# Performance work log

Hardware: AMD Instinct MI355X
Metric: run time of the kernel (lower is better)

The kernel has to match this reference:

```python
import jax, jax.numpy as jnp
import numpy as np

B, N, F, H, R = 16, 64, 64, 4, 50
C = F * H  # n_coefficients = n_heads * hidden_features
CUTOFF = 5.0  # ExpNormalSmearing cutoff_upper (cutoff_lower = 0)


def _dense(k, fin, fout):
    s = 1.0 / np.sqrt(fin)
    return jax.random.uniform(k, (fin, fout), jnp.float32, -s, s)


def setup_inputs() -> dict:
    key = jax.random.key(0)
    ks = jax.random.split(key, 20)
    start = float(np.exp(-CUTOFF))
    return {
        "h": jax.random.normal(ks[0], (B, N, F), jnp.float32),
        "x": jax.random.normal(ks[1], (B, N, 3), jnp.float32),
        "v": jax.random.normal(ks[2], (B, N, 3), jnp.float32) * 0.1,
        # edge model (ContinuousFilterConvolutionWithConcatenation)
        "W_in": _dense(ks[3], 2 * F, R), "b_in": jnp.zeros((R,), jnp.float32),
        "rbf_means": jnp.linspace(start, 1.0, R).astype(jnp.float32),
        "rbf_betas": jnp.full((R,), (2.0 / R * (1.0 - start)) ** -2, jnp.float32),
        "W_e1": _dense(ks[4], 2 * F + R + 1, F), "b_e1": jnp.zeros((F,), jnp.float32),
        "W_e2": _dense(ks[5], F, F), "b_e2": jnp.zeros((F,), jnp.float32),
        # semantic attention
        "W_sem": _dense(ks[6], F, H), "b_sem": jnp.zeros((H,), jnp.float32),
        "log_gamma": -jnp.log(jnp.linspace(1.0, 5.0, H)).astype(jnp.float32),
        # spatial attention
        "W_xmix": _dense(ks[7], C, C),
        "W_post1": _dense(ks[8], C, F), "b_post1": jnp.zeros((F,), jnp.float32),
        "W_post2": _dense(ks[9], F, F), "b_post2": jnp.zeros((F,), jnp.float32),
        # node update
        "W_node1": _dense(ks[10], F + C + F, F), "b_node1": jnp.zeros((F,), jnp.float32),
        "W_node2": _dense(ks[11], F, F), "b_node2": jnp.zeros((F,), jnp.float32),
        # velocity update
        "W_vel1": _dense(ks[12], F, F), "b_vel1": jnp.zeros((F,), jnp.float32),
        "W_vel2": _dense(ks[13], F, 1),
        "W_vmix": _dense(ks[14], C, 1),
    }


def reference(h, x, v, W_in, b_in, rbf_means, rbf_betas, W_e1, b_e1, W_e2, b_e2,
              W_sem, b_sem, log_gamma, W_xmix, W_post1, b_post1, W_post2, b_post2,
              W_node1, b_node1, W_node2, b_node2, W_vel1, b_vel1, W_vel2, W_vmix):
    silu = jax.nn.silu
    n = h.shape[-2]
    # pairwise displacement x_j - x_i : (B, N, N, 3)
    x_minus_xt = x[..., None, :, :] - x[..., :, None, :]
    d = jnp.sqrt(jax.nn.relu((x_minus_xt ** 2).sum(-1, keepdims=True)) + 1e-5)  # (B,N,N,1)
    # pairwise node features [h_j, h_i] : (B, N, N, 2F)
    hj = jnp.broadcast_to(h[..., None, :, :], h.shape[:-2] + (n, n, h.shape[-1]))
    hi = jnp.broadcast_to(h[..., :, None, :], hj.shape)
    h_cat = jnp.concatenate([hj, hi], -1)
    # edge model: RBF-smeared continuous-filter conv with concatenation
    h_mid = h_cat @ W_in + b_in  # (B,N,N,R)
    cut = 0.5 * (jnp.cos(d * (jnp.pi / CUTOFF)) + 1.0) * (d < CUTOFF)
    rbf = cut * jnp.exp(-rbf_betas * (jnp.exp(-d) - rbf_means) ** 2)  # (B,N,N,R)
    h_e = jnp.concatenate([h_cat, rbf * h_mid, d], -1)
    h_e = silu(h_e @ W_e1 + b_e1) @ W_e2 + b_e2  # (B,N,N,F)
    # attentions, softmax over neighbor axis (-2), diagonal masked out
    eye = jnp.eye(n, dtype=h.dtype)[:, :, None]
    sem = jax.nn.celu(h_e @ W_sem + b_sem, alpha=2.0) - 1e5 * eye
    sem = jax.nn.softmax(sem, axis=-2)  # (B,N,N,H)
    euc = jax.nn.softmax(-(d + 1e5 * eye) * jnp.exp(log_gamma), axis=-2)  # (B,N,N,H)
    att = euc * sem
    att = att / att.sum(-2, keepdims=True)
    # per-head attention-weighted edge features, flattened (F outer, H inner)
    h_e_att = (h_e[..., :, None] * att[..., None, :]).reshape(att.shape[:-1] + (F * H,))
    # spatial attention on unit displacement vectors
    coeff = jnp.tanh(h_e_att @ W_xmix)  # (B,N,N,C)
    x_hat = x_minus_xt / (d + 1e-5)
    comb = x_hat[..., None, :] * coeff[..., None]  # (B,N,N,C,3)
    comb_sum = comb.mean(axis=-3)  # mean over neighbors -> (B,N,C,3)
    h_comb = (comb_sum ** 2).sum(-1)  # invariant squared norms (B,N,C)
    h_comb = silu(silu(h_comb @ W_post1 + b_post1) @ W_post2 + b_post2)
    # node update (residual)
    h_agg = h_e_att.sum(axis=-2)  # (B,N,C)
    h_out = h + silu(silu(jnp.concatenate([h, h_agg, h_comb], -1) @ W_node1 + b_node1) @ W_node2 + b_node2)
    # equivariant velocity / coordinate update
    delta_v = jnp.einsum('...ijcd,c->...id', comb, W_vmix[:, 0]) / n  # v_mixing + mean over j
    gate = 2.0 * jax.nn.sigmoid(silu(h_out @ W_vel1 + b_vel1) @ W_vel2)  # double_sigmoid, (B,N,1)
    v_out = delta_v + gate * v
    x_out = x + v_out
    return h_out, x_out, v_out
```

## Files before the change

kernel.cpp:

```cpp
#include <hip/hip_runtime.h>
#include <math.h>

#define NB 16
#define NN 64
#define NF 64
#define NH 4
#define NR 50
#define NC 256

typedef __attribute__((ext_vector_type(8))) short short8;
typedef __attribute__((ext_vector_type(4))) float f32x4;

#define WS_WE1R 0
#define WS_WE2  4096
#define WS_WX   8192
#define MID_F   36864
#define E1_F    (MID_F + 131072)
#define HAGG_F  (E1_F + 131072)
#define COMB_F  (HAGG_F + 262144)

__device__ __forceinline__ float siluf(float x) { return x / (1.f + __expf(-x)); }
__device__ __forceinline__ float tanhfast(float x) { return 1.f - 2.f / (__expf(2.f * x) + 1.f); }

__device__ __forceinline__ short f2bfs(float f) {
    __bf16 b = (__bf16)f;
    union { __bf16 b; short s; } u; u.b = b; return u.s;
}
__device__ __forceinline__ float bf1(ushort u) {
    union { unsigned u; float f; } c; c.u = ((unsigned)u) << 16; return c.f;
}
__device__ __forceinline__ float bflo(unsigned u) {
    union { unsigned u; float f; } c; c.u = u << 16; return c.f;
}
__device__ __forceinline__ float bfhi(unsigned u) {
    union { unsigned u; float f; } c; c.u = u & 0xFFFF0000u; return c.f;
}

__device__ __forceinline__ float wave_max(float v) {
#pragma unroll
    for (int s = 32; s >= 1; s >>= 1) v = fmaxf(v, __shfl_xor(v, s));
    return v;
}
__device__ __forceinline__ float wave_sum(float v) {
#pragma unroll
    for (int s = 32; s >= 1; s >>= 1) v += __shfl_xor(v, s);
    return v;
}

__global__ __launch_bounds__(256)
void prep_kernel(const float* __restrict__ W_e1, const float* __restrict__ b_e1,
                 const float* __restrict__ W_e2, const float* __restrict__ W_xmix,
                 const float* __restrict__ h, const float* __restrict__ W_in,
                 const float* __restrict__ b_in,
                 short* __restrict__ wpack, float* __restrict__ mid, float* __restrict__ e1)
{
    int blk = blockIdx.x, t = threadIdx.x;
    if (blk < 36) {
        int s = blk * 256 + t;
        short8 val;
        if (s < 512) {
            int cl = s & 15, g = (s >> 4) & 3, q = s >> 6;
            int ks = q & 1, nt = q >> 1;
            int c = nt * 16 + cl, k0 = 32 * ks + 8 * g;
#pragma unroll
            for (int i = 0; i < 8; i++) {
                int kr = k0 + i;
                float f = (kr < 50) ? W_e1[(128 + kr) * NF + c] : (kr == 50 ? W_e1[178 * NF + c] : 0.f);
                val[i] = f2bfs(f);
            }
            *(short8*)(&wpack[WS_WE1R + s * 8]) = val;
        } else if (s < 1024) {
            int u = s - 512;
            int cl = u & 15, g = (u >> 4) & 3, q = u >> 6;
            int ks = q & 1, nt = q >> 1;
            int c = nt * 16 + cl, k0 = 32 * ks + 8 * g;
#pragma unroll
            for (int i = 0; i < 8; i++) val[i] = f2bfs(W_e2[(k0 + i) * NF + c]);
            *(short8*)(&wpack[WS_WE2 + u * 8]) = val;
        } else {
            int u = s - 1024;
            int cl = u & 15, g = (u >> 4) & 3, q = u >> 6;
            int ks = q & 7, wn = q >> 3;
            int c = (wn >> 2) * 64 + (wn & 3) * 16 + cl, k0 = 32 * ks + 8 * g;
#pragma unroll
            for (int i = 0; i < 8; i++) val[i] = f2bfs(W_xmix[(k0 + i) * NC + c]);
            *(short8*)(&wpack[WS_WX + u * 8]) = val;
        }
    } else {
        int node = blk - 36;
        __shared__ float s_hn[64];
        if (t < 64) s_hn[t] = h[node * NF + t];
        __syncthreads();
        if (t < 64) {
            float acc = 0.f;
#pragma unroll 8
            for (int k = 0; k < 64; k++) acc += s_hn[k] * W_e1[k * NF + t];
            e1[node * 128 + t] = acc;
        } else if (t < 128) {
            int f = t - 64;
            float acc = b_e1[f];
#pragma unroll 8
            for (int k = 0; k < 64; k++) acc += s_hn[k] * W_e1[(64 + k) * NF + f];
            e1[node * 128 + 64 + f] = acc;
        } else if (t < 178) {
            int r = t - 128;
            float acc = 0.f;
#pragma unroll 8
            for (int k = 0; k < 64; k++) acc += s_hn[k] * W_in[k * NR + r];
            mid[node * 128 + r] = acc;
        } else if (t >= 192 && t < 242) {
            int r = t - 192;
            float acc = b_in[r];
#pragma unroll 8
            for (int k = 0; k < 64; k++) acc += s_hn[k] * W_in[(64 + k) * NR + r];
            mid[node * 128 + 64 + r] = acc;
        }
    }
}

__global__ __launch_bounds__(256)
void sake_edge_kernel(
    const float* __restrict__ x,
    const float* __restrict__ mid, const float* __restrict__ e1,
    const float* __restrict__ rbf_means, const float* __restrict__ rbf_betas,
    const float* __restrict__ b_e2,
    const float* __restrict__ W_sem, const float* __restrict__ b_sem,
    const float* __restrict__ log_gamma,
    const short* __restrict__ wpack,
    float* __restrict__ hagg_g, float* __restrict__ comb_g)
{
    const int bi = blockIdx.x;
    const int b  = bi >> 6;
    const int i  = bi & 63;
    const int t  = threadIdx.x;
    const int w  = t >> 6, l = t & 63, lr = l & 15, lg = l >> 4;

    __shared__ __align__(16) short s_A[16 * 64 * 8];
    __shared__ short s_he[64 * 66];
    __shared__ float s_xhat[256];
    __shared__ float s_att[256];
    __shared__ float s_wsem[256];
    __shared__ float s_midi[52];

    const short8* A8  = (const short8*)s_A;
    short8*       A8w = (short8*)s_A;
    const short8* We1p = (const short8*)(wpack + WS_WE1R);
    const short8* We2p = (const short8*)(wpack + WS_WE2);
    const short8* Wxp  = (const short8*)(wpack + WS_WX);

    s_wsem[t] = W_sem[t];
    if (t < 50) s_midi[t] = mid[(b * 64 + i) * 128 + 64 + t];
    if (t < 64) {
        int j = t;
        float dx = x[(b * NN + j) * 3 + 0] - x[(b * NN + i) * 3 + 0];
        float dy = x[(b * NN + j) * 3 + 1] - x[(b * NN + i) * 3 + 1];
        float dz = x[(b * NN + j) * 3 + 2] - x[(b * NN + i) * 3 + 2];
        float d2 = dx * dx + dy * dy + dz * dz;
        float d  = sqrtf(fmaxf(d2, 0.f) + 1e-5f);
        float inv = 1.f / (d + 1e-5f);
        s_xhat[j * 4 + 0] = dx * inv;
        s_xhat[j * 4 + 1] = dy * inv;
        s_xhat[j * 4 + 2] = dz * inv;
        s_xhat[j * 4 + 3] = d;
    }
    __syncthreads();

    {
        int j = t & 63, p = t >> 6;
        float d = s_xhat[j * 4 + 3];
        float cut = 0.5f * (__cosf(d * 0.6283185307179586f) + 1.f) * (d < 5.f ? 1.f : 0.f);
        float emd = __expf(-d);
        const float* midj = mid + (b * 64 + j) * 128;
#pragma unroll
        for (int q = 0; q < 2; q++) {
            int sl = 2 * p + q;
            short8 val;
#pragma unroll
            for (int e = 0; e < 8; e++) {
                int r = sl * 8 + e;
                float o;
                if (r < 50) {
                    float m = midj[r] + s_midi[r];
                    float df = emd - rbf_means[r];
                    o = cut * __expf(-rbf_betas[r] * df * df) * m;
                } else if (r == 50) o = d;
                else o = 0.f;
                val[e] = f2bfs(o);
            }
            A8w[sl * 64 + j] = val;
        }
    }
    __syncthreads();

    {
        int f = w * 16 + lr;
        const float* e1b = e1 + (size_t)b * 64 * 128;
        float e1i_v = e1b[i * 128 + 64 + f];
        f32x4 acc[4];
#pragma unroll
        for (int jt = 0; jt < 4; jt++)
#pragma unroll
            for (int r = 0; r < 4; r++) {
                int j = jt * 16 + lg * 4 + r;
                acc[jt][r] = e1b[j * 128 + f] + e1i_v;
            }
#pragma unroll
        for (int ks = 0; ks < 2; ks++) {
            short8 bb = We1p[(w * 2 + ks) * 64 + l];
#pragma unroll
            for (int jt = 0; jt < 4; jt++) {
                short8 aa = A8[(ks * 4 + lg) * 64 + jt * 16 + lr];
                acc[jt] = __builtin_amdgcn_mfma_f32_16x16x32_bf16(aa, bb, acc[jt], 0, 0, 0);
            }
        }
        __syncthreads();
#pragma unroll
        for (int jt = 0; jt < 4; jt++)
#pragma unroll
            for (int r = 0; r < 4; r++) {
                int j = jt * 16 + lg * 4 + r;
                s_A[((f >> 3) * 64 + j) * 8 + (f & 7)] = f2bfs(siluf(acc[jt][r]));
            }
        __syncthreads();
    }

    {
        f32x4 acc[4];
#pragma unroll
        for (int jt = 0; jt < 4; jt++) { acc[jt][0] = 0.f; acc[jt][1] = 0.f; acc[jt][2] = 0.f; acc[jt][3] = 0.f; }
#pragma unroll
        for (int ks = 0; ks < 2; ks++) {
            short8 bb = We2p[(w * 2 + ks) * 64 + l];
#pragma unroll
            for (int jt = 0; jt < 4; jt++) {
                short8 aa = A8[(ks * 4 + lg) * 64 + jt * 16 + lr];
                acc[jt] = __builtin_amdgcn_mfma_f32_16x16x32_bf16(aa, bb, acc[jt], 0, 0, 0);
            }
        }
        float be2 = b_e2[w * 16 + lr];
        int f = w * 16 + lr;
#pragma unroll
        for (int jt = 0; jt < 4; jt++)
#pragma unroll
            for (int r = 0; r < 4; r++) {
                int j = jt * 16 + lg * 4 + r;
                s_he[j * 66 + f] = f2bfs(acc[jt][r] + be2);
            }
        __syncthreads();
    }

    {
        int hh = w, j = l;
        float acc = b_sem[hh];
        const unsigned* hp = (const unsigned*)(s_he + j * 66);
#pragma unroll 8
        for (int q = 0; q < 32; q++) {
            unsigned u = hp[q];
            acc += bflo(u) * s_wsem[(2 * q) * 4 + hh] + bfhi(u) * s_wsem[(2 * q + 1) * 4 + hh];
        }
        float cel = fmaxf(acc, 0.f) + fminf(0.f, 2.f * (__expf(0.5f * acc) - 1.f));
        float diag = (j == i) ? 1e5f : 0.f;
        float slog = cel - diag;
        float m1 = wave_max(slog);
        float e1v = __expf(slog - m1);
        float sem = e1v / wave_sum(e1v);
        float gam = __expf(log_gamma[hh]);
        float elog = -(s_xhat[j * 4 + 3] + diag) * gam;
        float m2 = wave_max(elog);
        float e2 = __expf(elog - m2);
        float euc = e2 / wave_sum(e2);
        float a = sem * euc;
        a = a / wave_sum(a);
        s_att[j * 4 + hh] = a;
    }
    __syncthreads();

    {
        int f = t >> 2, hh = t & 3;
        float acc = 0.f;
#pragma unroll 8
        for (int j = 0; j < 64; j++) acc += bf1((ushort)s_he[j * 66 + f]) * s_att[j * 4 + hh];
        hagg_g[bi * 256 + t] = acc;
    }

    f32x4 acc[4][4];
#pragma unroll
    for (int jt = 0; jt < 4; jt++)
#pragma unroll
        for (int nt = 0; nt < 4; nt++) { acc[jt][nt][0] = 0.f; acc[jt][nt][1] = 0.f; acc[jt][nt][2] = 0.f; acc[jt][nt][3] = 0.f; }

    for (int half = 0; half < 2; half++) {
        {
            int j = t & 63, kc = t >> 6;
            float a0 = s_att[j * 4 + 0], a1 = s_att[j * 4 + 1];
            float a2 = s_att[j * 4 + 2], a3 = s_att[j * 4 + 3];
#pragma unroll
            for (int s = 0; s < 4; s++) {
                int sl = kc * 4 + s;
                int kbase = half * 128 + sl * 8;
                unsigned u = *(const unsigned*)(s_he + j * 66 + (kbase >> 2));
                float h0 = bflo(u), h1 = bfhi(u);
                short8 val;
                val[0] = f2bfs(h0 * a0); val[1] = f2bfs(h0 * a1);
                val[2] = f2bfs(h0 * a2); val[3] = f2bfs(h0 * a3);
                val[4] = f2bfs(h1 * a0); val[5] = f2bfs(h1 * a1);
                val[6] = f2bfs(h1 * a2); val[7] = f2bfs(h1 * a3);
                A8w[sl * 64 + j] = val;
            }
        }
        __syncthreads();
#pragma unroll
        for (int ks = 0; ks < 4; ks++) {
            short8 aa[4], bb[4];
#pragma unroll
            for (int jt = 0; jt < 4; jt++) aa[jt] = A8[(ks * 4 + lg) * 64 + jt * 16 + lr];
#pragma unroll
            for (int nt = 0; nt < 4; nt++) bb[nt] = Wxp[((w * 4 + nt) * 8 + half * 4 + ks) * 64 + l];
#pragma unroll
            for (int jt = 0; jt < 4; jt++)
#pragma unroll
                for (int nt = 0; nt < 4; nt++)
                    acc[jt][nt] = __builtin_amdgcn_mfma_f32_16x16x32_bf16(aa[jt], bb[nt], acc[jt][nt], 0, 0, 0);
        }
        __syncthreads();
    }

    {
#pragma unroll
        for (int nt = 0; nt < 4; nt++) {
            float p0 = 0.f, p1 = 0.f, p2 = 0.f;
#pragma unroll
            for (int jt = 0; jt < 4; jt++)
#pragma unroll
                for (int r = 0; r < 4; r++) {
                    int j = jt * 16 + lg * 4 + r;
                    float th = tanhfast(acc[jt][nt][r]);
                    p0 += s_xhat[j * 4 + 0] * th;
                    p1 += s_xhat[j * 4 + 1] * th;
                    p2 += s_xhat[j * 4 + 2] * th;
                }
            p0 += __shfl_xor(p0, 16); p0 += __shfl_xor(p0, 32);
            p1 += __shfl_xor(p1, 16); p1 += __shfl_xor(p1, 32);
            p2 += __shfl_xor(p2, 16); p2 += __shfl_xor(p2, 32);
            if (lg == 0) {
                int c = w * 64 + nt * 16 + lr;
                float* cg = comb_g + bi * 768 + c * 3;
                cg[0] = p0 * (1.f / 64.f);
                cg[1] = p1 * (1.f / 64.f);
                cg[2] = p2 * (1.f / 64.f);
            }
        }
    }
}

__global__ __launch_bounds__(256)
void sake_tail_kernel(
    const float* __restrict__ h, const float* __restrict__ x, const float* __restrict__ v,
    const float* __restrict__ hagg_g, const float* __restrict__ comb_g,
    const float* __restrict__ W_post1, const float* __restrict__ b_post1,
    const float* __restrict__ W_post2, const float* __restrict__ b_post2,
    const float* __restrict__ W_node1, const float* __restrict__ b_node1,
    const float* __restrict__ W_node2, const float* __restrict__ b_node2,
    const float* __restrict__ W_vel1, const float* __restrict__ b_vel1,
    const float* __restrict__ W_vel2, const float* __restrict__ W_vmix,
    float* __restrict__ out_h, float* __restrict__ out_x, float* __restrict__ out_v)
{
    const int node = blockIdx.x;
    const int t = threadIdx.x, w = t >> 6, l = t & 63;

    __shared__ float s_in[384];
    __shared__ float s_hcp[256];
    __shared__ float s_cmb[3][256];
    __shared__ float s_red[4][64];
    __shared__ float s_vec[64];
    __shared__ float s_ho[64];

    {
        const float* cg = comb_g + node * 768;
        float c0 = cg[t * 3 + 0], c1 = cg[t * 3 + 1], c2 = cg[t * 3 + 2];
        s_cmb[0][t] = c0; s_cmb[1][t] = c1; s_cmb[2][t] = c2;
        s_hcp[t] = c0 * c0 + c1 * c1 + c2 * c2;
        if (t < 64) s_in[t] = h[node * NF + t];
        s_in[64 + t] = hagg_g[node * 256 + t];
    }
    __syncthreads();

    {
        float p = 0.f;
#pragma unroll 8
        for (int k = w * 64; k < w * 64 + 64; k++) p += s_hcp[k] * W_post1[k * NF + l];
        s_red[w][l] = p;
    }
    __syncthreads();
    {
        float a = b_post1[l] + s_red[0][l] + s_red[1][l] + s_red[2][l] + s_red[3][l];
        if (w == 0) s_vec[l] = siluf(a);
    }
    __syncthreads();

    {
        float p = 0.f;
#pragma unroll
        for (int k = w * 16; k < w * 16 + 16; k++) p += s_vec[k] * W_post2[k * NF + l];
        s_red[w][l] = p;
    }
    __syncthreads();
    {
        float a = b_post2[l] + s_red[0][l] + s_red[1][l] + s_red[2][l] + s_red[3][l];
        if (w == 0) s_in[320 + l] = siluf(a);
    }
    __syncthreads();

    {
        float p = 0.f;
#pragma unroll 8
        for (int k = w * 96; k < w * 96 + 96; k++) p += s_in[k] * W_node1[k * NF + l];
        s_red[w][l] = p;
    }
    __syncthreads();
    {
        float a = b_node1[l] + s_red[0][l] + s_red[1][l] + s_red[2][l] + s_red[3][l];
        if (w == 0) s_vec[l] = siluf(a);
    }
    __syncthreads();

    {
        float p = 0.f;
#pragma unroll
        for (int k = w * 16; k < w * 16 + 16; k++) p += s_vec[k] * W_node2[k * NF + l];
        s_red[w][l] = p;
    }
    __syncthreads();
    {
        float a = b_node2[l] + s_red[0][l] + s_red[1][l] + s_red[2][l] + s_red[3][l];
        float ho = s_in[l] + siluf(a);
        if (w == 0) { out_h[node * NF + l] = ho; s_ho[l] = ho; }
    }
    __syncthreads();

    {
        float p = 0.f;
#pragma unroll
        for (int k = w * 16; k < w * 16 + 16; k++) p += s_ho[k] * W_vel1[k * NF + l];
        s_red[w][l] = p;
    }
    __syncthreads();
    {
        float a = b_vel1[l] + s_red[0][l] + s_red[1][l] + s_red[2][l] + s_red[3][l];
        float v1 = siluf(a);
        float g = wave_sum(v1 * W_vel2[l]);
        g = 2.f / (1.f + __expf(-g));
        if (w < 3) {
            float pv = 0.f;
#pragma unroll
            for (int q = 0; q < 4; q++) pv += s_cmb[w][q * 64 + l] * W_vmix[q * 64 + l];
            float dv = wave_sum(pv);
            if (l == 0) {
                float vout = dv + g * v[node * 3 + w];
                out_v[node * 3 + w] = vout;
                out_x[node * 3 + w] = x[node * 3 + w] + vout;
            }
        }
    }
}

extern "C" void kernel_launch(void* const* d_in, const int* in_sizes, int n_in,
                              void* d_out, int out_size, void* d_ws, size_t ws_size,
                              hipStream_t stream) {
    const float* h        = (const float*)d_in[0];
    const float* x        = (const float*)d_in[1];
    const float* v        = (const float*)d_in[2];
    const float* W_in     = (const float*)d_in[3];
    const float* b_in     = (const float*)d_in[4];
    const float* rbf_m    = (const float*)d_in[5];
    const float* rbf_b    = (const float*)d_in[6];
    const float* W_e1     = (const float*)d_in[7];
    const float* b_e1     = (const float*)d_in[8];
    const float* W_e2     = (const float*)d_in[9];
    const float* b_e2     = (const float*)d_in[10];
    const float* W_sem    = (const float*)d_in[11];
    const float* b_sem    = (const float*)d_in[12];
    const float* log_g    = (const float*)d_in[13];
    const float* W_xmix   = (const float*)d_in[14];
    const float* W_post1  = (const float*)d_in[15];
    const float* b_post1  = (const float*)d_in[16];
    const float* W_post2  = (const float*)d_in[17];
    const float* b_post2  = (const float*)d_in[18];
    const float* W_node1  = (const float*)d_in[19];
    const float* b_node1  = (const float*)d_in[20];
    const float* W_node2  = (const float*)d_in[21];
    const float* b_node2  = (const float*)d_in[22];
    const float* W_vel1   = (const float*)d_in[23];
    const float* b_vel1   = (const float*)d_in[24];
    const float* W_vel2   = (const float*)d_in[25];
    const float* W_vmix   = (const float*)d_in[26];

    float* out   = (float*)d_out;
    float* out_h = out;
    float* out_x = out + NB * NN * NF;
    float* out_v = out + NB * NN * NF + NB * NN * 3;

    short* wpack = (short*)d_ws;
    float* wsf   = (float*)d_ws;
    float* mid   = wsf + MID_F;
    float* e1    = wsf + E1_F;
    float* hagg  = wsf + HAGG_F;
    float* comb  = wsf + COMB_F;

    prep_kernel<<<36 + 1024, 256, 0, stream>>>(W_e1, b_e1, W_e2, W_xmix, h, W_in, b_in,
                                               wpack, mid, e1);

    sake_edge_kernel<<<NB * NN, 256, 0, stream>>>(
        x, mid, e1, rbf_m, rbf_b, b_e2, W_sem, b_sem, log_g,
        wpack, hagg, comb);

    sake_tail_kernel<<<1024, 256, 0, stream>>>(
        h, x, v, hagg, comb,
        W_post1, b_post1, W_post2, b_post2, W_node1, b_node1, W_node2, b_node2,
        W_vel1, b_vel1, W_vel2, W_vmix, out_h, out_x, out_v);
}
```

Before: 56.05 us.

## Batch tail MLPs over 16 nodes with bf16 MFMA and transpose mid buffer

The tail kernel now processes 16 nodes per block and runs the post, node and velocity MLPs as bf16 MFMA matmuls on weights prepacked by the prep kernel, replacing per-node scalar fp32 dot products launched 1024 times. The mid buffer is stored transposed so edge blocks read it coalesced across j. The edge kernel also pads s_he rows to 72 for 16-byte vector reads, drops one barrier by writing the first-layer activations into a separate region of s_A, and splits the hagg reduction over two lanes. In exchange, the tail MLPs lose precision by going to bf16, and the tail launch has only 64 blocks.

```diff
diff --git a/kernel.cpp b/kernel.cpp
--- a/kernel.cpp
+++ b/kernel.cpp
@@ -14,7 +14,12 @@
 #define WS_WE1R 0
 #define WS_WE2  4096
 #define WS_WX   8192
-#define MID_F   36864
+#define WS_PO1  73728
+#define WS_NO1  90112
+#define WS_PO2  114688
+#define WS_NO2  118784
+#define WS_VE1  122880
+#define MID_F   65536
 #define E1_F    (MID_F + 131072)
 #define HAGG_F  (E1_F + 131072)
 #define COMB_F  (HAGG_F + 262144)
@@ -50,12 +55,15 @@
 __global__ __launch_bounds__(256)
 void prep_kernel(const float* __restrict__ W_e1, const float* __restrict__ b_e1,
                  const float* __restrict__ W_e2, const float* __restrict__ W_xmix,
+                 const float* __restrict__ W_post1, const float* __restrict__ W_node1,
+                 const float* __restrict__ W_post2, const float* __restrict__ W_node2,
+                 const float* __restrict__ W_vel1,
                  const float* __restrict__ h, const float* __restrict__ W_in,
                  const float* __restrict__ b_in,
-                 short* __restrict__ wpack, float* __restrict__ mid, float* __restrict__ e1)
+                 short* __restrict__ wpack, float* __restrict__ mid_T, float* __restrict__ e1)
 {
     int blk = blockIdx.x, t = threadIdx.x;
-    if (blk < 36) {
+    if (blk < 62) {
         int s = blk * 256 + t;
         short8 val;
         if (s < 512) {
@@ -77,7 +85,7 @@
 #pragma unroll
             for (int i = 0; i < 8; i++) val[i] = f2bfs(W_e2[(k0 + i) * NF + c]);
             *(short8*)(&wpack[WS_WE2 + u * 8]) = val;
-        } else {
+        } else if (s < 9216) {
             int u = s - 1024;
             int cl = u & 15, g = (u >> 4) & 3, q = u >> 6;
             int ks = q & 7, wn = q >> 3;
@@ -85,9 +93,49 @@
 #pragma unroll
             for (int i = 0; i < 8; i++) val[i] = f2bfs(W_xmix[(k0 + i) * NC + c]);
             *(short8*)(&wpack[WS_WX + u * 8]) = val;
+        } else if (s < 11264) {
+            int u = s - 9216;
+            int cl = u & 15, g = (u >> 4) & 3, q = u >> 6;
+            int ks = q & 7, nt = q >> 3;
+            int c = nt * 16 + cl, k0 = 32 * ks + 8 * g;
+#pragma unroll
+            for (int i = 0; i < 8; i++) val[i] = f2bfs(W_post1[(k0 + i) * NF + c]);
+            *(short8*)(&wpack[WS_PO1 + u * 8]) = val;
+        } else if (s < 14336) {
+            int u = s - 11264;
+            int cl = u & 15, g = (u >> 4) & 3, q = u >> 6;
+            int ks = q % 12, nt = q / 12;
+            int c = nt * 16 + cl, k0 = 32 * ks + 8 * g;
+#pragma unroll
+            for (int i = 0; i < 8; i++) val[i] = f2bfs(W_node1[(k0 + i) * NF + c]);
+            *(short8*)(&wpack[WS_NO1 + u * 8]) = val;
+        } else if (s < 14848) {
+            int u = s - 14336;
+            int cl = u & 15, g = (u >> 4) & 3, q = u >> 6;
+            int ks = q & 1, nt = q >> 1;
+            int c = nt * 16 + cl, k0 = 32 * ks + 8 * g;
+#pragma unroll
+            for (int i = 0; i < 8; i++) val[i] = f2bfs(W_post2[(k0 + i) * NF + c]);
+            *(short8*)(&wpack[WS_PO2 + u * 8]) = val;
+        } else if (s < 15360) {
+            int u = s - 14848;
+            int cl = u & 15, g = (u >> 4) & 3, q = u >> 6;
+            int ks = q & 1, nt = q >> 1;
+            int c = nt * 16 + cl, k0 = 32 * ks + 8 * g;
+#pragma unroll
+            for (int i = 0; i < 8; i++) val[i] = f2bfs(W_node2[(k0 + i) * NF + c]);
+            *(short8*)(&wpack[WS_NO2 + u * 8]) = val;
+        } else {
+            int u = s - 15360;
+            int cl = u & 15, g = (u >> 4) & 3, q = u >> 6;
+            int ks = q & 1, nt = q >> 1;
+            int c = nt * 16 + cl, k0 = 32 * ks + 8 * g;
+#pragma unroll
+            for (int i = 0; i < 8; i++) val[i] = f2bfs(W_vel1[(k0 + i) * NF + c]);
+            *(short8*)(&wpack[WS_VE1 + u * 8]) = val;
         }
     } else {
-        int node = blk - 36;
+        int node = blk - 62;
         __shared__ float s_hn[64];
         if (t < 64) s_hn[t] = h[node * NF + t];
         __syncthreads();
@@ -107,13 +155,13 @@
             float acc = 0.f;
 #pragma unroll 8
             for (int k = 0; k < 64; k++) acc += s_hn[k] * W_in[k * NR + r];
-            mid[node * 128 + r] = acc;
+            mid_T[r * 1024 + node] = acc;
         } else if (t >= 192 && t < 242) {
             int r = t - 192;
             float acc = b_in[r];
 #pragma unroll 8
             for (int k = 0; k < 64; k++) acc += s_hn[k] * W_in[(64 + k) * NR + r];
-            mid[node * 128 + 64 + r] = acc;
+            mid_T[(64 + r) * 1024 + node] = acc;
         }
     }
 }
@@ -121,7 +169,7 @@
 __global__ __launch_bounds__(256)
 void sake_edge_kernel(
     const float* __restrict__ x,
-    const float* __restrict__ mid, const float* __restrict__ e1,
+    const float* __restrict__ mid_T, const float* __restrict__ e1,
     const float* __restrict__ rbf_means, const float* __restrict__ rbf_betas,
     const float* __restrict__ b_e2,
     const float* __restrict__ W_sem, const float* __restrict__ b_sem,
@@ -136,7 +184,7 @@
     const int w  = t >> 6, l = t & 63, lr = l & 15, lg = l >> 4;
 
     __shared__ __align__(16) short s_A[16 * 64 * 8];
-    __shared__ short s_he[64 * 66];
+    __shared__ __align__(16) short s_he[64 * 72];
     __shared__ float s_xhat[256];
     __shared__ float s_att[256];
     __shared__ float s_wsem[256];
@@ -149,7 +197,7 @@
     const short8* Wxp  = (const short8*)(wpack + WS_WX);
 
     s_wsem[t] = W_sem[t];
-    if (t < 50) s_midi[t] = mid[(b * 64 + i) * 128 + 64 + t];
+    if (t < 50) s_midi[t] = mid_T[(64 + t) * 1024 + b * 64 + i];
     if (t < 64) {
         int j = t;
         float dx = x[(b * NN + j) * 3 + 0] - x[(b * NN + i) * 3 + 0];
@@ -170,7 +218,7 @@
         float d = s_xhat[j * 4 + 3];
         float cut = 0.5f * (__cosf(d * 0.6283185307179586f) + 1.f) * (d < 5.f ? 1.f : 0.f);
         float emd = __expf(-d);
-        const float* midj = mid + (b * 64 + j) * 128;
+        const float* mcol = mid_T + b * 64 + j;
 #pragma unroll
         for (int q = 0; q < 2; q++) {
             int sl = 2 * p + q;
@@ -180,7 +228,7 @@
                 int r = sl * 8 + e;
                 float o;
                 if (r < 50) {
-                    float m = midj[r] + s_midi[r];
+                    float m = mcol[r * 1024] + s_midi[r];
                     float df = emd - rbf_means[r];
                     o = cut * __expf(-rbf_betas[r] * df * df) * m;
                 } else if (r == 50) o = d;
@@ -213,13 +261,12 @@
                 acc[jt] = __builtin_amdgcn_mfma_f32_16x16x32_bf16(aa, bb, acc[jt], 0, 0, 0);
             }
         }
-        __syncthreads();
 #pragma unroll
         for (int jt = 0; jt < 4; jt++)
 #pragma unroll
             for (int r = 0; r < 4; r++) {
                 int j = jt * 16 + lg * 4 + r;
-                s_A[((f >> 3) * 64 + j) * 8 + (f & 7)] = f2bfs(siluf(acc[jt][r]));
+                s_A[(((f >> 3) + 8) * 64 + j) * 8 + (f & 7)] = f2bfs(siluf(acc[jt][r]));
             }
         __syncthreads();
     }
@@ -233,7 +280,7 @@
             short8 bb = We2p[(w * 2 + ks) * 64 + l];
 #pragma unroll
             for (int jt = 0; jt < 4; jt++) {
-                short8 aa = A8[(ks * 4 + lg) * 64 + jt * 16 + lr];
+                short8 aa = A8[((8 + ks * 4 + lg)) * 64 + jt * 16 + lr];
                 acc[jt] = __builtin_amdgcn_mfma_f32_16x16x32_bf16(aa, bb, acc[jt], 0, 0, 0);
             }
         }
@@ -244,19 +291,21 @@
 #pragma unroll
             for (int r = 0; r < 4; r++) {
                 int j = jt * 16 + lg * 4 + r;
-                s_he[j * 66 + f] = f2bfs(acc[jt][r] + be2);
+                s_he[j * 72 + f] = f2bfs(acc[jt][r] + be2);
             }
         __syncthreads();
     }
 
     {
         int hh = w, j = l;
+        const short8* hrow = (const short8*)(s_he + j * 72);
         float acc = b_sem[hh];
-        const unsigned* hp = (const unsigned*)(s_he + j * 66);
-#pragma unroll 8
-        for (int q = 0; q < 32; q++) {
-            unsigned u = hp[q];
-            acc += bflo(u) * s_wsem[(2 * q) * 4 + hh] + bfhi(u) * s_wsem[(2 * q + 1) * 4 + hh];
+#pragma unroll
+        for (int q = 0; q < 8; q++) {
+            short8 hv = hrow[q];
+#pragma unroll
+            for (int e = 0; e < 8; e++)
+                acc += bf1((ushort)hv[e]) * s_wsem[(q * 8 + e) * 4 + hh];
         }
         float cel = fmaxf(acc, 0.f) + fminf(0.f, 2.f * (__expf(0.5f * acc) - 1.f));
         float diag = (j == i) ? 1e5f : 0.f;
@@ -276,11 +325,22 @@
     __syncthreads();
 
     {
-        int f = t >> 2, hh = t & 3;
-        float acc = 0.f;
+        int f2 = t >> 3, hh = (t >> 1) & 3, jh = t & 1;
+        float a0 = 0.f, a1 = 0.f;
 #pragma unroll 8
-        for (int j = 0; j < 64; j++) acc += bf1((ushort)s_he[j * 66 + f]) * s_att[j * 4 + hh];
-        hagg_g[bi * 256 + t] = acc;
+        for (int jj = 0; jj < 32; jj++) {
+            int j = jh * 32 + jj;
+            float at = s_att[j * 4 + hh];
+            unsigned u = *(const unsigned*)(s_he + j * 72 + 2 * f2);
+            a0 += bflo(u) * at;
+            a1 += bfhi(u) * at;
+        }
+        a0 += __shfl_xor(a0, 1);
+        a1 += __shfl_xor(a1, 1);
+        if (!jh) {
+            hagg_g[bi * 256 + (2 * f2) * 4 + hh]     = a0;
+            hagg_g[bi * 256 + (2 * f2 + 1) * 4 + hh] = a1;
+        }
     }
 
     f32x4 acc[4][4];
@@ -294,12 +354,11 @@
             int j = t & 63, kc = t >> 6;
             float a0 = s_att[j * 4 + 0], a1 = s_att[j * 4 + 1];
             float a2 = s_att[j * 4 + 2], a3 = s_att[j * 4 + 3];
+            short8 hv = *(const short8*)(s_he + j * 72 + (half * 32 + kc * 8));
 #pragma unroll
             for (int s = 0; s < 4; s++) {
                 int sl = kc * 4 + s;
-                int kbase = half * 128 + sl * 8;
-                unsigned u = *(const unsigned*)(s_he + j * 66 + (kbase >> 2));
-                float h0 = bflo(u), h1 = bfhi(u);
+                float h0 = bf1((ushort)hv[2 * s]), h1 = bf1((ushort)hv[2 * s + 1]);
                 short8 val;
                 val[0] = f2bfs(h0 * a0); val[1] = f2bfs(h0 * a1);
                 val[2] = f2bfs(h0 * a2); val[3] = f2bfs(h0 * a3);
@@ -357,109 +416,175 @@
 void sake_tail_kernel(
     const float* __restrict__ h, const float* __restrict__ x, const float* __restrict__ v,
     const float* __restrict__ hagg_g, const float* __restrict__ comb_g,
-    const float* __restrict__ W_post1, const float* __restrict__ b_post1,
-    const float* __restrict__ W_post2, const float* __restrict__ b_post2,
-    const float* __restrict__ W_node1, const float* __restrict__ b_node1,
-    const float* __restrict__ W_node2, const float* __restrict__ b_node2,
-    const float* __restrict__ W_vel1, const float* __restrict__ b_vel1,
+    const float* __restrict__ b_post1, const float* __restrict__ b_post2,
+    const float* __restrict__ b_node1, const float* __restrict__ b_node2,
+    const float* __restrict__ b_vel1,
     const float* __restrict__ W_vel2, const float* __restrict__ W_vmix,
+    const short* __restrict__ wpack,
     float* __restrict__ out_h, float* __restrict__ out_x, float* __restrict__ out_v)
 {
-    const int node = blockIdx.x;
-    const int t = threadIdx.x, w = t >> 6, l = t & 63;
-
-    __shared__ float s_in[384];
-    __shared__ float s_hcp[256];
-    __shared__ float s_cmb[3][256];
-    __shared__ float s_red[4][64];
-    __shared__ float s_vec[64];
-    __shared__ float s_ho[64];
-
-    {
-        const float* cg = comb_g + node * 768;
-        float c0 = cg[t * 3 + 0], c1 = cg[t * 3 + 1], c2 = cg[t * 3 + 2];
-        s_cmb[0][t] = c0; s_cmb[1][t] = c1; s_cmb[2][t] = c2;
-        s_hcp[t] = c0 * c0 + c1 * c1 + c2 * c2;
-        if (t < 64) s_in[t] = h[node * NF + t];
-        s_in[64 + t] = hagg_g[node * 256 + t];
+    const int g0 = blockIdx.x * 16;
+    const int t = threadIdx.x;
+    const int w = t >> 6, l = t & 63, lr = l & 15, lg = l >> 4;
+
+    __shared__ __align__(16) short s_Aa[88 * 16 * 8];
+    __shared__ float s_wv[256];
+    __shared__ float s_wv2[64];
+    __shared__ float s_red[4][16];
+
+    const short8* A8  = (const short8*)s_Aa;
+    const short8* PO1p = (const short8*)(wpack + WS_PO1);
+    const short8* NO1p = (const short8*)(wpack + WS_NO1);
+    const short8* PO2p = (const short8*)(wpack + WS_PO2);
+    const short8* NO2p = (const short8*)(wpack + WS_NO2);
+    const short8* VE1p = (const short8*)(wpack + WS_VE1);
+
+    {
+        s_wv[t] = W_vmix[t];
+        if (t < 64) s_wv2[t] = W_vel2[t];
+        int n = t & 15, c0 = (t >> 4) * 16;
+        const float* cg = comb_g + (g0 + n) * 768;
+        const float* ha = hagg_g + (g0 + n) * 256;
+#pragma unroll
+        for (int cc = 0; cc < 16; cc++) {
+            int c = c0 + cc;
+            float v0 = cg[c * 3 + 0], v1 = cg[c * 3 + 1], v2 = cg[c * 3 + 2];
+            float hcp = v0 * v0 + v1 * v1 + v2 * v2;
+            s_Aa[((c >> 3) * 16 + n) * 8 + (c & 7)] = f2bfs(hcp);
+            s_Aa[((40 + (c >> 3)) * 16 + n) * 8 + (c & 7)] = f2bfs(ha[c]);
+        }
+        int f0 = (t >> 4) * 4;
+#pragma unroll
+        for (int ff = 0; ff < 4; ff++) {
+            int f = f0 + ff;
+            s_Aa[((32 + (f >> 3)) * 16 + n) * 8 + (f & 7)] = f2bfs(h[(g0 + n) * 64 + f]);
+        }
     }
     __syncthreads();
 
     {
-        float p = 0.f;
-#pragma unroll 8
-        for (int k = w * 64; k < w * 64 + 64; k++) p += s_hcp[k] * W_post1[k * NF + l];
-        s_red[w][l] = p;
-    }
-    __syncthreads();
-    {
-        float a = b_post1[l] + s_red[0][l] + s_red[1][l] + s_red[2][l] + s_red[3][l];
-        if (w == 0) s_vec[l] = siluf(a);
-    }
-    __syncthreads();
-
-    {
-        float p = 0.f;
-#pragma unroll
-        for (int k = w * 16; k < w * 16 + 16; k++) p += s_vec[k] * W_post2[k * NF + l];
-        s_red[w][l] = p;
-    }
-    __syncthreads();
-    {
-        float a = b_post2[l] + s_red[0][l] + s_red[1][l] + s_red[2][l] + s_red[3][l];
-        if (w == 0) s_in[320 + l] = siluf(a);
-    }
-    __syncthreads();
-
-    {
-        float p = 0.f;
-#pragma unroll 8
-        for (int k = w * 96; k < w * 96 + 96; k++) p += s_in[k] * W_node1[k * NF + l];
-        s_red[w][l] = p;
-    }
-    __syncthreads();
-    {
-        float a = b_node1[l] + s_red[0][l] + s_red[1][l] + s_red[2][l] + s_red[3][l];
-        if (w == 0) s_vec[l] = siluf(a);
-    }
-    __syncthreads();
-
-    {
-        float p = 0.f;
-#pragma unroll
-        for (int k = w * 16; k < w * 16 + 16; k++) p += s_vec[k] * W_node2[k * NF + l];
-        s_red[w][l] = p;
-    }
-    __syncthreads();
-    {
-        float a = b_node2[l] + s_red[0][l] + s_red[1][l] + s_red[2][l] + s_red[3][l];
-        float ho = s_in[l] + siluf(a);
-        if (w == 0) { out_h[node * NF + l] = ho; s_ho[l] = ho; }
-    }
-    __syncthreads();
-
-    {
-        float p = 0.f;
-#pragma unroll
-        for (int k = w * 16; k < w * 16 + 16; k++) p += s_ho[k] * W_vel1[k * NF + l];
-        s_red[w][l] = p;
-    }
-    __syncthreads();
-    {
-        float a = b_vel1[l] + s_red[0][l] + s_red[1][l] + s_red[2][l] + s_red[3][l];
-        float v1 = siluf(a);
-        float g = wave_sum(v1 * W_vel2[l]);
-        g = 2.f / (1.f + __expf(-g));
-        if (w < 3) {
-            float pv = 0.f;
-#pragma unroll
-            for (int q = 0; q < 4; q++) pv += s_cmb[w][q * 64 + l] * W_vmix[q * 64 + l];
-            float dv = wave_sum(pv);
-            if (l == 0) {
-                float vout = dv + g * v[node * 3 + w];
-                out_v[node * 3 + w] = vout;
-                out_x[node * 3 + w] = x[node * 3 + w] + vout;
-            }
+        f32x4 acc = {0.f, 0.f, 0.f, 0.f};
+#pragma unroll
+        for (int ks = 0; ks < 8; ks++) {
+            short8 aa = A8[(ks * 4 + lg) * 16 + lr];
+            short8 bb = PO1p[((w * 8 + ks) * 4 + lg) * 16 + lr];
+            acc = __builtin_amdgcn_mfma_f32_16x16x32_bf16(aa, bb, acc, 0, 0, 0);
+        }
+        int f = w * 16 + lr;
+        float bp = b_post1[f];
+        __syncthreads();
+#pragma unroll
+        for (int r = 0; r < 4; r++) {
+            int n = lg * 4 + r;
+            s_Aa[((80 + (f >> 3)) * 16 + n) * 8 + (f & 7)] = f2bfs(siluf(acc[r] + bp));
+        }
+        __syncthreads();
+    }
+
+    {
+        f32x4 acc = {0.f, 0.f, 0.f, 0.f};
+#pragma unroll
+        for (int ks = 0; ks < 2; ks++) {
+            short8 aa = A8[((80 + ks * 4 + lg)) * 16 + lr];
+            short8 bb = PO2p[((w * 2 + ks) * 4 + lg) * 16 + lr];
+            acc = __builtin_amdgcn_mfma_f32_16x16x32_bf16(aa, bb, acc, 0, 0, 0);
+        }
+        int f = w * 16 + lr;
+        float bp = b_post2[f];
+#pragma unroll
+        for (int r = 0; r < 4; r++) {
+            int n = lg * 4 + r;
+            s_Aa[((72 + (f >> 3)) * 16 + n) * 8 + (f & 7)] = f2bfs(siluf(acc[r] + bp));
+        }
+        __syncthreads();
+    }
+
+    {
+        f32x4 acc = {0.f, 0.f, 0.f, 0.f};
+#pragma unroll
+        for (int ks = 0; ks < 12; ks++) {
+            short8 aa = A8[((32 + ks * 4 + lg)) * 16 + lr];
+            short8 bb = NO1p[((w * 12 + ks) * 4 + lg) * 16 + lr];
+            acc = __builtin_amdgcn_mfma_f32_16x16x32_bf16(aa, bb, acc, 0, 0, 0);
+        }
+        int f = w * 16 + lr;
+        float bp = b_node1[f];
+#pragma unroll
+        for (int r = 0; r < 4; r++) {
+            int n = lg * 4 + r;
+            s_Aa[((f >> 3) * 16 + n) * 8 + (f & 7)] = f2bfs(siluf(acc[r] + bp));
+        }
+        __syncthreads();
+    }
+
+    {
+        f32x4 acc = {0.f, 0.f, 0.f, 0.f};
+#pragma unroll
+        for (int ks = 0; ks < 2; ks++) {
+            short8 aa = A8[(ks * 4 + lg) * 16 + lr];
+            short8 bb = NO2p[((w * 2 + ks) * 4 + lg) * 16 + lr];
+            acc = __builtin_amdgcn_mfma_f32_16x16x32_bf16(aa, bb, acc, 0, 0, 0);
+        }
+        int f = w * 16 + lr;
+        float bp = b_node2[f];
+#pragma unroll
+        for (int r = 0; r < 4; r++) {
+            int n = lg * 4 + r;
+            float ho = h[(g0 + n) * 64 + f] + siluf(acc[r] + bp);
+            out_h[(g0 + n) * 64 + f] = ho;
+            s_Aa[((8 + (f >> 3)) * 16 + n) * 8 + (f & 7)] = f2bfs(ho);
+        }
+        __syncthreads();
+    }
+
+    {
+        f32x4 acc = {0.f, 0.f, 0.f, 0.f};
+#pragma unroll
+        for (int ks = 0; ks < 2; ks++) {
+            short8 aa = A8[((8 + ks * 4 + lg)) * 16 + lr];
+            short8 bb = VE1p[((w * 2 + ks) * 4 + lg) * 16 + lr];
+            acc = __builtin_amdgcn_mfma_f32_16x16x32_bf16(aa, bb, acc, 0, 0, 0);
+        }
+        int f = w * 16 + lr;
+        float bp = b_vel1[f];
+        float wv2 = s_wv2[f];
+#pragma unroll
+        for (int r = 0; r < 4; r++) {
+            float p = siluf(acc[r] + bp) * wv2;
+            p += __shfl_xor(p, 1); p += __shfl_xor(p, 2);
+            p += __shfl_xor(p, 4); p += __shfl_xor(p, 8);
+            if (lr == 0) s_red[w][lg * 4 + r] = p;
+        }
+        __syncthreads();
+    }
+
+    {
+        int n = t >> 4, q = t & 15;
+        float p0 = 0.f, p1 = 0.f, p2 = 0.f;
+        const float* cg = comb_g + (g0 + n) * 768;
+#pragma unroll
+        for (int cc = 0; cc < 16; cc++) {
+            int c = q * 16 + cc;
+            float wv = s_wv[c];
+            p0 += cg[c * 3 + 0] * wv;
+            p1 += cg[c * 3 + 1] * wv;
+            p2 += cg[c * 3 + 2] * wv;
+        }
+        p0 += __shfl_xor(p0, 1); p0 += __shfl_xor(p0, 2); p0 += __shfl_xor(p0, 4); p0 += __shfl_xor(p0, 8);
+        p1 += __shfl_xor(p1, 1); p1 += __shfl_xor(p1, 2); p1 += __shfl_xor(p1, 4); p1 += __shfl_xor(p1, 8);
+        p2 += __shfl_xor(p2, 1); p2 += __shfl_xor(p2, 2); p2 += __shfl_xor(p2, 4); p2 += __shfl_xor(p2, 8);
+        if (q == 0) {
+            float g = s_red[0][n] + s_red[1][n] + s_red[2][n] + s_red[3][n];
+            g = 2.f / (1.f + __expf(-g));
+            float dv0 = p0 + g * v[(g0 + n) * 3 + 0];
+            float dv1 = p1 + g * v[(g0 + n) * 3 + 1];
+            float dv2 = p2 + g * v[(g0 + n) * 3 + 2];
+            out_v[(g0 + n) * 3 + 0] = dv0;
+            out_v[(g0 + n) * 3 + 1] = dv1;
+            out_v[(g0 + n) * 3 + 2] = dv2;
+            out_x[(g0 + n) * 3 + 0] = x[(g0 + n) * 3 + 0] + dv0;
+            out_x[(g0 + n) * 3 + 1] = x[(g0 + n) * 3 + 1] + dv1;
+            out_x[(g0 + n) * 3 + 2] = x[(g0 + n) * 3 + 2] + dv2;
         }
     }
 }
@@ -502,20 +627,21 @@
 
     short* wpack = (short*)d_ws;
     float* wsf   = (float*)d_ws;
-    float* mid   = wsf + MID_F;
+    float* mid_T = wsf + MID_F;
     float* e1    = wsf + E1_F;
     float* hagg  = wsf + HAGG_F;
     float* comb  = wsf + COMB_F;
 
-    prep_kernel<<<36 + 1024, 256, 0, stream>>>(W_e1, b_e1, W_e2, W_xmix, h, W_in, b_in,
-                                               wpack, mid, e1);
+    prep_kernel<<<62 + 1024, 256, 0, stream>>>(
+        W_e1, b_e1, W_e2, W_xmix, W_post1, W_node1, W_post2, W_node2, W_vel1,
+        h, W_in, b_in, wpack, mid_T, e1);
 
     sake_edge_kernel<<<NB * NN, 256, 0, stream>>>(
-        x, mid, e1, rbf_m, rbf_b, b_e2, W_sem, b_sem, log_g,
+        x, mid_T, e1, rbf_m, rbf_b, b_e2, W_sem, b_sem, log_g,
         wpack, hagg, comb);
 
-    sake_tail_kernel<<<1024, 256, 0, stream>>>(
+    sake_tail_kernel<<<64, 256, 0, stream>>>(
         h, x, v, hagg, comb,
-        W_post1, b_post1, W_post2, b_post2, W_node1, b_node1, W_node2, b_node2,
-        W_vel1, b_vel1, W_vel2, W_vmix, out_h, out_x, out_v);
-}
+        b_post1, b_post2, b_node1, b_node2, b_vel1,
+        W_vel2, W_vmix, wpack, out_h, out_x, out_v);
+}
```

Measured after the change: 58.16 us. +3.8%, slower.
